# Performance work log

Hardware: AMD Instinct MI355X
Metric: run time of the kernel (lower is better)

Reference implementation:

```python
import jax, jax.numpy as jnp
import numpy as np


def setup_inputs() -> dict:
    key = jax.random.key(0)
    ks = jax.random.split(key, 5)
    B, H, W, C = 4, 64, 64, 256
    Ck = C // 8  # key/query channels = 32
    x = jax.random.normal(ks[0], (B, H, W, C), dtype=jnp.float32)
    # 1x1 conv kernels (spec_norm=False -> plain conv), Glorot-ish scaling
    Wf = jax.random.normal(ks[1], (C, Ck), dtype=jnp.float32) * (1.0 / np.sqrt(C))
    Wg = jax.random.normal(ks[2], (C, Ck), dtype=jnp.float32) * (1.0 / np.sqrt(C))
    Wh = jax.random.normal(ks[3], (C, C), dtype=jnp.float32) * (1.0 / np.sqrt(C))
    bf = jnp.zeros((Ck,), dtype=jnp.float32)
    bg = jnp.zeros((Ck,), dtype=jnp.float32)
    bh = jnp.zeros((C,), dtype=jnp.float32)
    # gamma is zero-init in the module; use a nonzero value so the attention
    # branch actually contributes to the output (as after some training).
    gamma = jnp.float32(0.5)
    return {"x": x, "Wf": Wf, "bf": bf, "Wg": Wg, "bg": bg,
            "Wh": Wh, "bh": bh, "gamma": gamma}


def reference(x, Wf, bf, Wg, bg, Wh, bh, gamma):
    B, H, W, C = x.shape
    N = H * W
    xf = x.reshape(B, N, C)  # hw_flatten of input (1x1 conv == per-pixel matmul)
    f = xf @ Wf + bf         # [B, N, Ck] keys
    g = xf @ Wg + bg         # [B, N, Ck] queries
    h = xf @ Wh + bh         # [B, N, C]  values
    s = jnp.einsum('bqk,bnk->bqn', g, f)  # [B, N, N] scores (g @ f^T)
    b = jax.nn.softmax(s, axis=-1)
    o = jnp.einsum('bqn,bnc->bqc', b, h)  # [B, N, C]
    # in-channels == nfilters, so scale(x) = x (identity)
    y = gamma * o.reshape(B, H, W, C) + x
    return y
```

## Files before the change

### kernel.cpp

```cpp
#include <hip/hip_runtime.h>
#include <stdint.h>

#define B_ 4
#define N_ 4096
#define C_ 256
#define LOG2E 1.44269504088896340736f
#define SOFT_OFF 88.0f

typedef float f32x4 __attribute__((ext_vector_type(4)));
typedef float f32x16 __attribute__((ext_vector_type(16)));
typedef short s16x8 __attribute__((ext_vector_type(8)));
typedef __bf16 bf16x8 __attribute__((ext_vector_type(8)));
typedef _Float16 f16x8 __attribute__((ext_vector_type(8)));

static __device__ __forceinline__ unsigned short f2bf(float f) {
    union { float f; uint32_t u; } v; v.f = f;
    return (unsigned short)((v.u + 0x7FFFu + ((v.u >> 16) & 1u)) >> 16);
}
static __device__ __forceinline__ unsigned short f2bf_rh(float f) {
    union { float f; uint32_t u; } v; v.f = f;
    return (unsigned short)((v.u + 0x8000u) >> 16);
}

__global__ __launch_bounds__(256) void wprep(
    const float* __restrict__ Wf, const float* __restrict__ Wg,
    const float* __restrict__ Wh, _Float16* __restrict__ WT)
{
    __shared__ float tile[64][33];
    const int t = blockIdx.x, kc = blockIdx.y, tid = threadIdx.x;
    const float* src; int stride;
    if (t == 0)      { src = Wf;                stride = 32;  }
    else if (t == 1) { src = Wg;                stride = 32;  }
    else             { src = Wh + (t - 2) * 32; stride = 256; }

    const int c = tid & 31, a = tid >> 5;
    #pragma unroll
    for (int p = 0; p < 8; p++) {
        int kk = p * 8 + a;
        tile[kk][c] = src[(size_t)(kc * 64 + kk) * stride + c];
    }
    __syncthreads();
    const int kk = tid & 63, aa = tid >> 6;
    #pragma unroll
    for (int p = 0; p < 8; p++) {
        int cc = p * 4 + aa;
        WT[(size_t)(t * 32 + cc) * 256 + kc * 64 + kk] = (_Float16)tile[kk][cc];
    }
}

__global__ __launch_bounds__(256, 2) void proj_kernel(
    const float* __restrict__ x,
    const float* __restrict__ bfp, const float* __restrict__ bgp,
    const float* __restrict__ bhp,
    const _Float16* __restrict__ WT,
    _Float16* __restrict__ qf16, _Float16* __restrict__ kf16,
    unsigned short* __restrict__ v_frag)
{
    __shared__ __align__(16) _Float16 xs[64 * 256];
    __shared__ __align__(16) unsigned short tbuf[4][32 * 40];

    const int tid  = threadIdx.x;
    const int lane = tid & 63;
    const int wave = tid >> 6;
    const int m_   = lane & 31;
    const int k8   = lane >> 5;
    const int row0 = blockIdx.x * 64;
    const int half = blockIdx.y;
    const int b    = row0 >> 12;
    const int n0   = row0 & 4095;
    const int kt   = n0 >> 6;

    #pragma unroll
    for (int i = 0; i < 8; i++) {
        int r  = 8 * i + (tid >> 5);
        int c5 = tid & 31;
        const f32x4* src = (const f32x4*)(x + (size_t)(row0 + r) * 256 + c5 * 8);
        f32x4 a = src[0], c4 = src[1];
        f16x8 h = { (_Float16)a.x, (_Float16)a.y, (_Float16)a.z, (_Float16)a.w,
                    (_Float16)c4.x, (_Float16)c4.y, (_Float16)c4.z, (_Float16)c4.w };
        int chunk = (((r >> 5) * 32 + c5)) * 32 + ((r & 31) ^ (c5 & 7));
        *(f16x8*)(xs + chunk * 8) = h;
    }
    __syncthreads();

    const int rowsub = wave & 1;
    const int tg     = wave >> 1;
    const int ntile  = (half == 0) ? 3 : 2;
    const int t_base = (half == 0) ? tg * 3 : 6 + tg * 2;
    const _Float16* wb[3];
    #pragma unroll
    for (int t = 0; t < 3; t++)
        wb[t] = WT + (size_t)((t_base + (t < ntile ? t : 0)) * 32 + m_) * 256 + k8 * 8;

    f32x16 acc[3];
    #pragma unroll
    for (int t = 0; t < 3; t++)
        #pragma unroll
        for (int i = 0; i < 16; i++) acc[t][i] = 0.f;

    f16x8 Bb[2][4][3];
    #pragma unroll
    for (int j = 0; j < 4; j++)
        #pragma unroll
        for (int t = 0; t < 3; t++) {
            if (t >= ntile) break;
            Bb[0][j][t] = *(const f16x8*)(wb[t] + j * 16);
        }
    #pragma unroll
    for (int g4 = 0; g4 < 4; g4++) {
        const int cur = g4 & 1, nxt = cur ^ 1;
        if (g4 < 3)
            #pragma unroll
            for (int j = 0; j < 4; j++)
                #pragma unroll
                for (int t = 0; t < 3; t++) {
                    if (t >= ntile) break;
                    Bb[nxt][j][t] = *(const f16x8*)(wb[t] + (g4 * 4 + 4 + j) * 16);
                }
        #pragma unroll
        for (int j = 0; j < 4; j++) {
            int ks = g4 * 4 + j;
            f16x8 A = *(const f16x8*)(xs + ((rowsub * 32 + ks * 2 + k8) * 32
                                            + (m_ ^ ((ks * 2 + k8) & 7))) * 8);
            #pragma unroll
            for (int t = 0; t < 3; t++) {
                if (t >= ntile) break;
                acc[t] = __builtin_amdgcn_mfma_f32_32x32x16_f16(A, Bb[cur][j][t],
                                                                acc[t], 0, 0, 0);
            }
        }
    }

    #pragma unroll
    for (int t = 0; t < 3; t++) {
        if (t >= ntile) break;
        const int tile = t_base + t;
        if (tile < 2) {
            float bias = (tile == 0) ? bfp[m_] : bgp[m_];
            _Float16* dst = (tile == 0) ? kf16 : qf16;
            #pragma unroll
            for (int r = 0; r < 16; r++) {
                int m = (r & 3) + 8 * (r >> 2) + 4 * k8;
                int row = row0 + rowsub * 32 + m;
                dst[(size_t)row * 32 + m_] = (_Float16)(acc[t][r] + bias);
            }
        } else {
            const int ht   = tile - 2;
            const int chgv = ht >> 2, chslv = ht & 3;
            float bias = bhp[ht * 32 + m_];
            unsigned short* buf = tbuf[wave];
            #pragma unroll
            for (int u = 0; u < 8; u++) {
                int r = 2 * u;
                int m = (r & 3) + 8 * (r >> 2) + 4 * k8;
                uint32_t v = (uint32_t)f2bf(acc[t][r] + bias)
                           | ((uint32_t)f2bf(acc[t][r + 1] + bias) << 16);
                *(uint32_t*)(buf + m_ * 40 + m) = v;
            }
            #pragma unroll
            for (int u = 0; u < 2; u++) {
                int idx2 = u * 64 + lane;
                int chr = idx2 >> 2, q8 = idx2 & 3;
                s16x8 vv = *(const s16x8*)(buf + chr * 40 + q8 * 8);
                int oct = rowsub * 4 + q8;
                size_t e = (((((size_t)(b * 2 + chgv) * 64 + kt) * 8 + oct) * 4
                              + chslv) * 32 + chr) * 8;
                *(s16x8*)(v_frag + e) = vv;
            }
        }
    }
}

__global__ __launch_bounds__(1024, 4) void attn_kernel(
    const _Float16* __restrict__ qf16, const _Float16* __restrict__ kf16,
    const unsigned short* __restrict__ v_frag,
    const float* __restrict__ x, const float* __restrict__ gamma_p,
    float* __restrict__ out)
{
    __shared__ __align__(16) unsigned short P_s[2][2][4096];
    __shared__ float l_s[2][4][32];

    const int tid  = threadIdx.x;
    const int lane = tid & 63;
    const int wave = tid >> 6;
    const int qsub = wave & 1;
    const int j    = wave >> 1;
    const int m_   = lane & 31;
    const int k8   = lane >> 5;
    const int qt   = blockIdx.x;
    const int b    = blockIdx.y;
    const size_t bn = (size_t)b * N_;
    const bool is_s = (wave < 8);
    const int ksl  = j;
    const int octw = ksl * 4 + (m_ >> 3);
    const int osw  = octw & 3;
    const int kofs = m_ & 7;

    const unsigned short* vb = v_frag + (size_t)(b * 2 + (j >> 2)) * 524288
                             + (j & 3) * 256 + m_ * 8;

    const int qrow = qt * 64 + qsub * 32 + m_;
    const f16x8 Aq0 = *(const f16x8*)(qf16 + (bn + qrow) * 32 + k8 * 8);
    const f16x8 Aq1 = *(const f16x8*)(qf16 + (bn + qrow) * 32 + 16 + k8 * 8);

    f16x8 Kc0 = {}, Kc1 = {};
    if (is_s) {
        const _Float16* kp = kf16 + (bn + ksl * 32 + m_) * 32;
        Kc0 = *(const f16x8*)(kp + k8 * 8);
        Kc1 = *(const f16x8*)(kp + 16 + k8 * 8);
    }
    bf16x8 Bv0[4], Bv1[4];
    #pragma unroll
    for (int ks = 0; ks < 4; ks++)
        Bv0[ks] = *(const bf16x8*)(vb + (ks * 2 + k8) * 1024);

    f32x16 acc;
    float l_acc[16];
    #pragma unroll
    for (int i = 0; i < 16; i++) { acc[i] = 0.f; l_acc[i] = 0.f; }

    for (int it = 0; it < 32; it++) {
        const int par = it & 1;
        const int itn = (it < 31) ? it + 1 : 31;
        f16x8 Kn0 = {}, Kn1 = {};
        if (is_s) {
            const _Float16* kp = kf16 + (bn + itn * 128 + ksl * 32 + m_) * 32;
            Kn0 = *(const f16x8*)(kp + k8 * 8);
            Kn1 = *(const f16x8*)(kp + 16 + k8 * 8);
            f32x16 s;
            #pragma unroll
            for (int i = 0; i < 16; i++) s[i] = 0.f;
            s = __builtin_amdgcn_mfma_f32_32x32x16_f16(Aq0, Kc0, s, 0, 0, 0);
            s = __builtin_amdgcn_mfma_f32_32x32x16_f16(Aq1, Kc1, s, 0, 0, 0);
            unsigned short* Pb = P_s[par][qsub];
            #pragma unroll
            for (int r = 0; r < 16; r++) {
                float p = __builtin_amdgcn_exp2f(fmaf(s[r], LOG2E, -SOFT_OFF));
                l_acc[r] += p;
                int q = (r & 3) + 8 * (r >> 2) + 4 * k8;
                Pb[(octw * 32 + (q ^ osw)) * 8 + kofs] = f2bf_rh(p);
            }
        }
        __syncthreads();

        const unsigned short* Pr = P_s[par][qsub];
        #pragma unroll
        for (int ks = 0; ks < 4; ks++)
            Bv1[ks] = *(const bf16x8*)(vb + (size_t)it * 16384 + 8192
                                       + (ks * 2 + k8) * 1024);
        #pragma unroll
        for (int ks = 0; ks < 4; ks++) {
            int oct = ks * 2 + k8;
            bf16x8 Ap = *(const bf16x8*)(Pr + (oct * 32 + (m_ ^ (oct & 3))) * 8);
            acc = __builtin_amdgcn_mfma_f32_32x32x16_bf16(Ap, Bv0[ks], acc, 0, 0, 0);
        }
        #pragma unroll
        for (int ks = 0; ks < 4; ks++) {
            int oct = 8 + ks * 2 + k8;
            bf16x8 Ap = *(const bf16x8*)(Pr + (oct * 32 + (m_ ^ (oct & 3))) * 8);
            acc = __builtin_amdgcn_mfma_f32_32x32x16_bf16(Ap, Bv1[ks], acc, 0, 0, 0);
        }
        #pragma unroll
        for (int ks = 0; ks < 4; ks++)
            Bv0[ks] = *(const bf16x8*)(vb + (size_t)itn * 16384
                                       + (ks * 2 + k8) * 1024);
        if (is_s) { Kc0 = Kn0; Kc1 = Kn1; }
    }

    if (is_s) {
        #pragma unroll
        for (int off = 1; off < 32; off <<= 1)
            #pragma unroll
            for (int r = 0; r < 16; r++)
                l_acc[r] += __shfl_xor(l_acc[r], off, 64);
        if (m_ == 0) {
            #pragma unroll
            for (int r = 0; r < 16; r++) {
                int q = (r & 3) + 8 * (r >> 2) + 4 * k8;
                l_s[qsub][ksl][q] = l_acc[r];
            }
        }
    }
    __syncthreads();

    const float gamma = *gamma_p;
    #pragma unroll
    for (int r = 0; r < 16; r++) {
        int q = (r & 3) + 8 * (r >> 2) + 4 * k8;
        float l = l_s[qsub][0][q] + l_s[qsub][1][q]
                + l_s[qsub][2][q] + l_s[qsub][3][q];
        size_t idx = (bn + qt * 64 + qsub * 32 + q) * 256 + j * 32 + m_;
        out[idx] = gamma * (acc[r] / l) + x[idx];
    }
}

extern "C" void kernel_launch(void* const* d_in, const int* in_sizes, int n_in,
                              void* d_out, int out_size, void* d_ws, size_t ws_size,
                              hipStream_t stream) {
    const float* x   = (const float*)d_in[0];
    const float* Wf  = (const float*)d_in[1];
    const float* bfp = (const float*)d_in[2];
    const float* Wg  = (const float*)d_in[3];
    const float* bgp = (const float*)d_in[4];
    const float* Wh  = (const float*)d_in[5];
    const float* bhp = (const float*)d_in[6];
    const float* gam = (const float*)d_in[7];
    float* out = (float*)d_out;

    unsigned char* ws = (unsigned char*)d_ws;
    const size_t MB = 1 << 20;
    _Float16* WT    = (_Float16*)(ws);
    _Float16* qf16  = (_Float16*)(ws + 1 * MB);
    _Float16* kf16  = (_Float16*)(ws + 2 * MB);
    unsigned short* v_frag = (unsigned short*)(ws + 3 * MB);

    wprep<<<dim3(10, 4), dim3(256), 0, stream>>>(Wf, Wg, Wh, WT);
    proj_kernel<<<dim3(256, 2), dim3(256), 0, stream>>>(
        x, bfp, bgp, bhp, WT, qf16, kf16, v_frag);
    attn_kernel<<<dim3(64, 4), dim3(1024), 0, stream>>>(
        qf16, kf16, v_frag, x, gam, out);
}
```

Baseline: 149.8 us.

## Software-pipeline score computation one tile ahead, alternating between two wave groups

Score/exp work for the next key tile now runs while the PV MFMAs for the current tile execute. It writes into the other half of the double-buffered P tile, with a prologue that precomputes tile 0. The score duty alternates between the two 8-wave groups, so all 16 waves share the exp work instead of only the first 8. The row-sum reduction is extended to all waves with a vectorized layout. The aim is to hide the score/softmax latency behind the PV matmul and balance load across waves, at the cost of more complex index logic and a K prefetch two tiles ahead.

```diff
diff --git a/kernel.cpp b/kernel.cpp
--- a/kernel.cpp
+++ b/kernel.cpp
@@ -178,20 +178,20 @@
     float* __restrict__ out)
 {
     __shared__ __align__(16) unsigned short P_s[2][2][4096];
-    __shared__ float l_s[2][4][32];
+    __shared__ __align__(16) float l_s[2][32][8];
 
     const int tid  = threadIdx.x;
     const int lane = tid & 63;
     const int wave = tid >> 6;
     const int qsub = wave & 1;
     const int j    = wave >> 1;
+    const int ksl  = j & 3;
+    const int sgrp = j >> 2;
     const int m_   = lane & 31;
     const int k8   = lane >> 5;
     const int qt   = blockIdx.x;
     const int b    = blockIdx.y;
     const size_t bn = (size_t)b * N_;
-    const bool is_s = (wave < 8);
-    const int ksl  = j;
     const int octw = ksl * 4 + (m_ >> 3);
     const int osw  = octw & 3;
     const int kofs = m_ & 7;
@@ -203,9 +203,30 @@
     const f16x8 Aq0 = *(const f16x8*)(qf16 + (bn + qrow) * 32 + k8 * 8);
     const f16x8 Aq1 = *(const f16x8*)(qf16 + (bn + qrow) * 32 + 16 + k8 * 8);
 
-    f16x8 Kc0 = {}, Kc1 = {};
-    if (is_s) {
-        const _Float16* kp = kf16 + (bn + ksl * 32 + m_) * 32;
+    const _Float16* kp0 = kf16 + (bn + sgrp * 128 + ksl * 32 + m_) * 32;
+    f16x8 Kc0 = *(const f16x8*)(kp0 + k8 * 8);
+    f16x8 Kc1 = *(const f16x8*)(kp0 + 16 + k8 * 8);
+
+    f32x16 acc;
+    float l_acc[16];
+    #pragma unroll
+    for (int i = 0; i < 16; i++) { acc[i] = 0.f; l_acc[i] = 0.f; }
+
+    if (sgrp == 0) {
+        f32x16 s;
+        #pragma unroll
+        for (int i = 0; i < 16; i++) s[i] = 0.f;
+        s = __builtin_amdgcn_mfma_f32_32x32x16_f16(Aq0, Kc0, s, 0, 0, 0);
+        s = __builtin_amdgcn_mfma_f32_32x32x16_f16(Aq1, Kc1, s, 0, 0, 0);
+        unsigned short* Pb = P_s[0][qsub];
+        #pragma unroll
+        for (int r = 0; r < 16; r++) {
+            float p = __builtin_amdgcn_exp2f(fmaf(s[r], LOG2E, -SOFT_OFF));
+            l_acc[r] += p;
+            int q = (r & 3) + 8 * (r >> 2) + 4 * k8;
+            Pb[(octw * 32 + (q ^ osw)) * 8 + kofs] = f2bf_rh(p);
+        }
+        const _Float16* kp = kf16 + (bn + 2 * 128 + ksl * 32 + m_) * 32;
         Kc0 = *(const f16x8*)(kp + k8 * 8);
         Kc1 = *(const f16x8*)(kp + 16 + k8 * 8);
     }
@@ -213,26 +234,36 @@
     #pragma unroll
     for (int ks = 0; ks < 4; ks++)
         Bv0[ks] = *(const bf16x8*)(vb + (ks * 2 + k8) * 1024);
-
-    f32x16 acc;
-    float l_acc[16];
-    #pragma unroll
-    for (int i = 0; i < 16; i++) { acc[i] = 0.f; l_acc[i] = 0.f; }
+    __syncthreads();
 
     for (int it = 0; it < 32; it++) {
         const int par = it & 1;
         const int itn = (it < 31) ? it + 1 : 31;
-        f16x8 Kn0 = {}, Kn1 = {};
-        if (is_s) {
-            const _Float16* kp = kf16 + (bn + itn * 128 + ksl * 32 + m_) * 32;
-            Kn0 = *(const f16x8*)(kp + k8 * 8);
-            Kn1 = *(const f16x8*)(kp + 16 + k8 * 8);
-            f32x16 s;
+        const bool duty = (((it + 1) & 1) == sgrp) && (it < 31);
+
+        #pragma unroll
+        for (int ks = 0; ks < 4; ks++)
+            Bv1[ks] = *(const bf16x8*)(vb + (size_t)it * 16384 + 8192
+                                       + (ks * 2 + k8) * 1024);
+
+        f32x16 s;
+        if (duty) {
             #pragma unroll
             for (int i = 0; i < 16; i++) s[i] = 0.f;
             s = __builtin_amdgcn_mfma_f32_32x32x16_f16(Aq0, Kc0, s, 0, 0, 0);
             s = __builtin_amdgcn_mfma_f32_32x32x16_f16(Aq1, Kc1, s, 0, 0, 0);
-            unsigned short* Pb = P_s[par][qsub];
+        }
+
+        const unsigned short* Pr = P_s[par][qsub];
+        #pragma unroll
+        for (int ks = 0; ks < 4; ks++) {
+            int oct = ks * 2 + k8;
+            bf16x8 Ap = *(const bf16x8*)(Pr + (oct * 32 + (m_ ^ (oct & 3))) * 8);
+            acc = __builtin_amdgcn_mfma_f32_32x32x16_bf16(Ap, Bv0[ks], acc, 0, 0, 0);
+        }
+
+        if (duty) {
+            unsigned short* Pb = P_s[par ^ 1][qsub];
             #pragma unroll
             for (int r = 0; r < 16; r++) {
                 float p = __builtin_amdgcn_exp2f(fmaf(s[r], LOG2E, -SOFT_OFF));
@@ -240,20 +271,12 @@
                 int q = (r & 3) + 8 * (r >> 2) + 4 * k8;
                 Pb[(octw * 32 + (q ^ osw)) * 8 + kofs] = f2bf_rh(p);
             }
-        }
-        __syncthreads();
-
-        const unsigned short* Pr = P_s[par][qsub];
-        #pragma unroll
-        for (int ks = 0; ks < 4; ks++)
-            Bv1[ks] = *(const bf16x8*)(vb + (size_t)it * 16384 + 8192
-                                       + (ks * 2 + k8) * 1024);
-        #pragma unroll
-        for (int ks = 0; ks < 4; ks++) {
-            int oct = ks * 2 + k8;
-            bf16x8 Ap = *(const bf16x8*)(Pr + (oct * 32 + (m_ ^ (oct & 3))) * 8);
-            acc = __builtin_amdgcn_mfma_f32_32x32x16_bf16(Ap, Bv0[ks], acc, 0, 0, 0);
-        }
+            int kt3 = (it + 3 < 32) ? (it + 3) : 31;
+            const _Float16* kp = kf16 + (bn + (size_t)kt3 * 128 + ksl * 32 + m_) * 32;
+            Kc0 = *(const f16x8*)(kp + k8 * 8);
+            Kc1 = *(const f16x8*)(kp + 16 + k8 * 8);
+        }
+
         #pragma unroll
         for (int ks = 0; ks < 4; ks++) {
             int oct = 8 + ks * 2 + k8;
@@ -264,21 +287,19 @@
         for (int ks = 0; ks < 4; ks++)
             Bv0[ks] = *(const bf16x8*)(vb + (size_t)itn * 16384
                                        + (ks * 2 + k8) * 1024);
-        if (is_s) { Kc0 = Kn0; Kc1 = Kn1; }
-    }
-
-    if (is_s) {
-        #pragma unroll
-        for (int off = 1; off < 32; off <<= 1)
-            #pragma unroll
-            for (int r = 0; r < 16; r++)
-                l_acc[r] += __shfl_xor(l_acc[r], off, 64);
-        if (m_ == 0) {
-            #pragma unroll
-            for (int r = 0; r < 16; r++) {
-                int q = (r & 3) + 8 * (r >> 2) + 4 * k8;
-                l_s[qsub][ksl][q] = l_acc[r];
-            }
+        __syncthreads();
+    }
+
+    #pragma unroll
+    for (int off = 1; off < 32; off <<= 1)
+        #pragma unroll
+        for (int r = 0; r < 16; r++)
+            l_acc[r] += __shfl_xor(l_acc[r], off, 64);
+    if (m_ == 0) {
+        #pragma unroll
+        for (int r = 0; r < 16; r++) {
+            int q = (r & 3) + 8 * (r >> 2) + 4 * k8;
+            l_s[qsub][q][j] = l_acc[r];
         }
     }
     __syncthreads();
@@ -287,8 +308,10 @@
     #pragma unroll
     for (int r = 0; r < 16; r++) {
         int q = (r & 3) + 8 * (r >> 2) + 4 * k8;
-        float l = l_s[qsub][0][q] + l_s[qsub][1][q]
-                + l_s[qsub][2][q] + l_s[qsub][3][q];
+        f32x4 la = *(const f32x4*)(&l_s[qsub][q][0]);
+        f32x4 lb = *(const f32x4*)(&l_s[qsub][q][4]);
+        float l = ((la.x + la.y) + (la.z + la.w))
+                + ((lb.x + lb.y) + (lb.z + lb.w));
         size_t idx = (bn + qt * 64 + qsub * 32 + q) * 256 + j * 32 + m_;
         out[idx] = gamma * (acc[r] / l) + x[idx];
     }
```

Measured after the change: 176.3 us. 1.18x slower.

## Keep softmax probabilities in registers via transposed score MFMA, split keys across waves

Applied to the files above, without the earlier changes.

The attention kernel now computes S^T (K as the A operand) so each lane's exponentiated scores map directly onto the A-fragment layout of the PV MFMA. This removes the LDS round trip for P and the per-iteration __syncthreads. Each wave owns a key slice and accumulates 4 channel tiles, and the partial outputs are reduced across the 4 key-slice waves through LDS at the end. Blocks shrink to 512 threads covering 32 queries, and the V fragment write layout in the projection kernel is permuted to match the new operand ordering. The costs are more accumulator registers per wave, a serialized end-of-kernel reduction with several barriers, and lower occupancy.

```diff
diff --git a/kernel.cpp b/kernel.cpp
--- a/kernel.cpp
+++ b/kernel.cpp
@@ -9,6 +9,7 @@
 
 typedef float f32x4 __attribute__((ext_vector_type(4)));
 typedef float f32x16 __attribute__((ext_vector_type(16)));
+typedef short s16x4 __attribute__((ext_vector_type(4)));
 typedef short s16x8 __attribute__((ext_vector_type(8)));
 typedef __bf16 bf16x8 __attribute__((ext_vector_type(8)));
 typedef _Float16 f16x8 __attribute__((ext_vector_type(8)));
@@ -160,9 +161,13 @@
             #pragma unroll
             for (int u = 0; u < 2; u++) {
                 int idx2 = u * 64 + lane;
-                int chr = idx2 >> 2, q8 = idx2 & 3;
-                s16x8 vv = *(const s16x8*)(buf + chr * 40 + q8 * 8);
-                int oct = rowsub * 4 + q8;
+                int chr = idx2 >> 2, sl = idx2 & 3;
+                int gg = sl >> 1, hh = sl & 1;
+                s16x4 lo = *(const s16x4*)(buf + chr * 40 + gg * 16 + hh * 4);
+                s16x4 hi = *(const s16x4*)(buf + chr * 40 + gg * 16 + hh * 4 + 8);
+                s16x8 vv = { lo[0], lo[1], lo[2], lo[3],
+                             hi[0], hi[1], hi[2], hi[3] };
+                int oct = rowsub * 4 + sl;
                 size_t e = (((((size_t)(b * 2 + chgv) * 64 + kt) * 8 + oct) * 4
                               + chslv) * 32 + chr) * 8;
                 *(s16x8*)(v_frag + e) = vv;
@@ -171,126 +176,143 @@
     }
 }
 
-__global__ __launch_bounds__(1024, 4) void attn_kernel(
+__global__ __launch_bounds__(512, 2) void attn_kernel(
     const _Float16* __restrict__ qf16, const _Float16* __restrict__ kf16,
     const unsigned short* __restrict__ v_frag,
     const float* __restrict__ x, const float* __restrict__ gamma_p,
     float* __restrict__ out)
 {
-    __shared__ __align__(16) unsigned short P_s[2][2][4096];
-    __shared__ float l_s[2][4][32];
+    __shared__ __align__(16) float acc_s[32][256];
+    __shared__ float l_sl[4][32];
 
     const int tid  = threadIdx.x;
     const int lane = tid & 63;
     const int wave = tid >> 6;
-    const int qsub = wave & 1;
-    const int j    = wave >> 1;
+    const int ks   = wave & 3;
+    const int cg   = wave >> 2;
     const int m_   = lane & 31;
     const int k8   = lane >> 5;
     const int qt   = blockIdx.x;
-    const int b    = blockIdx.y;
+    const int qsub = blockIdx.y;
+    const int b    = blockIdx.z;
     const size_t bn = (size_t)b * N_;
-    const bool is_s = (wave < 8);
-    const int ksl  = j;
-    const int octw = ksl * 4 + (m_ >> 3);
-    const int osw  = octw & 3;
-    const int kofs = m_ & 7;
-
-    const unsigned short* vb = v_frag + (size_t)(b * 2 + (j >> 2)) * 524288
-                             + (j & 3) * 256 + m_ * 8;
 
     const int qrow = qt * 64 + qsub * 32 + m_;
     const f16x8 Aq0 = *(const f16x8*)(qf16 + (bn + qrow) * 32 + k8 * 8);
     const f16x8 Aq1 = *(const f16x8*)(qf16 + (bn + qrow) * 32 + 16 + k8 * 8);
 
-    f16x8 Kc0 = {}, Kc1 = {};
-    if (is_s) {
-        const _Float16* kp = kf16 + (bn + ksl * 32 + m_) * 32;
-        Kc0 = *(const f16x8*)(kp + k8 * 8);
-        Kc1 = *(const f16x8*)(kp + 16 + k8 * 8);
-    }
-    bf16x8 Bv0[4], Bv1[4];
-    #pragma unroll
-    for (int ks = 0; ks < 4; ks++)
-        Bv0[ks] = *(const bf16x8*)(vb + (ks * 2 + k8) * 1024);
-
-    f32x16 acc;
-    float l_acc[16];
-    #pragma unroll
-    for (int i = 0; i < 16; i++) { acc[i] = 0.f; l_acc[i] = 0.f; }
+    const _Float16* kbase = kf16 + (bn + ks * 32 + m_) * 32;
+    f16x8 Kc0 = *(const f16x8*)(kbase + k8 * 8);
+    f16x8 Kc1 = *(const f16x8*)(kbase + 16 + k8 * 8);
+
+    const unsigned short* vb = v_frag + (size_t)(b * 2 + cg) * 524288 + m_ * 8;
+    const int oct0 = ks * 4 + k8, oct1 = ks * 4 + 2 + k8;
+    const int off0 = (oct0 >> 3) * 8192 + (oct0 & 7) * 1024;
+    const int off1 = (oct1 >> 3) * 8192 + (oct1 & 7) * 1024;
+
+    f32x16 acc[4];
+    #pragma unroll
+    for (int t = 0; t < 4; t++)
+        #pragma unroll
+        for (int i = 0; i < 16; i++) acc[t][i] = 0.f;
+    float l_acc = 0.f;
 
     for (int it = 0; it < 32; it++) {
-        const int par = it & 1;
-        const int itn = (it < 31) ? it + 1 : 31;
-        f16x8 Kn0 = {}, Kn1 = {};
-        if (is_s) {
-            const _Float16* kp = kf16 + (bn + itn * 128 + ksl * 32 + m_) * 32;
-            Kn0 = *(const f16x8*)(kp + k8 * 8);
-            Kn1 = *(const f16x8*)(kp + 16 + k8 * 8);
-            f32x16 s;
-            #pragma unroll
-            for (int i = 0; i < 16; i++) s[i] = 0.f;
-            s = __builtin_amdgcn_mfma_f32_32x32x16_f16(Aq0, Kc0, s, 0, 0, 0);
-            s = __builtin_amdgcn_mfma_f32_32x32x16_f16(Aq1, Kc1, s, 0, 0, 0);
-            unsigned short* Pb = P_s[par][qsub];
-            #pragma unroll
-            for (int r = 0; r < 16; r++) {
-                float p = __builtin_amdgcn_exp2f(fmaf(s[r], LOG2E, -SOFT_OFF));
-                l_acc[r] += p;
-                int q = (r & 3) + 8 * (r >> 2) + 4 * k8;
-                Pb[(octw * 32 + (q ^ osw)) * 8 + kofs] = f2bf_rh(p);
-            }
+        const unsigned short* vit = vb + (size_t)it * 16384;
+        bf16x8 Bv0[4];
+        #pragma unroll
+        for (int t = 0; t < 4; t++)
+            Bv0[t] = *(const bf16x8*)(vit + t * 256 + off0);
+
+        f32x16 s2;
+        #pragma unroll
+        for (int i = 0; i < 16; i++) s2[i] = 0.f;
+        s2 = __builtin_amdgcn_mfma_f32_32x32x16_f16(Kc0, Aq0, s2, 0, 0, 0);
+        s2 = __builtin_amdgcn_mfma_f32_32x32x16_f16(Kc1, Aq1, s2, 0, 0, 0);
+
+        bf16x8 Bv1[4];
+        #pragma unroll
+        for (int t = 0; t < 4; t++)
+            Bv1[t] = *(const bf16x8*)(vit + t * 256 + off1);
+
+        {
+            int itn = (it < 31) ? it + 1 : 31;
+            Kc0 = *(const f16x8*)(kbase + itn * 4096 + k8 * 8);
+            Kc1 = *(const f16x8*)(kbase + itn * 4096 + 16 + k8 * 8);
+        }
+
+        float p0 = __builtin_amdgcn_exp2f(fmaf(s2[0], LOG2E, -SOFT_OFF));
+        float p1 = __builtin_amdgcn_exp2f(fmaf(s2[1], LOG2E, -SOFT_OFF));
+        float p2 = __builtin_amdgcn_exp2f(fmaf(s2[2], LOG2E, -SOFT_OFF));
+        float p3 = __builtin_amdgcn_exp2f(fmaf(s2[3], LOG2E, -SOFT_OFF));
+        float p4 = __builtin_amdgcn_exp2f(fmaf(s2[4], LOG2E, -SOFT_OFF));
+        float p5 = __builtin_amdgcn_exp2f(fmaf(s2[5], LOG2E, -SOFT_OFF));
+        float p6 = __builtin_amdgcn_exp2f(fmaf(s2[6], LOG2E, -SOFT_OFF));
+        float p7 = __builtin_amdgcn_exp2f(fmaf(s2[7], LOG2E, -SOFT_OFF));
+        l_acc += ((p0 + p1) + (p2 + p3)) + ((p4 + p5) + (p6 + p7));
+        union { uint32_t u[4]; bf16x8 v; } f0;
+        f0.u[0] = (uint32_t)f2bf_rh(p0) | ((uint32_t)f2bf_rh(p1) << 16);
+        f0.u[1] = (uint32_t)f2bf_rh(p2) | ((uint32_t)f2bf_rh(p3) << 16);
+        f0.u[2] = (uint32_t)f2bf_rh(p4) | ((uint32_t)f2bf_rh(p5) << 16);
+        f0.u[3] = (uint32_t)f2bf_rh(p6) | ((uint32_t)f2bf_rh(p7) << 16);
+        #pragma unroll
+        for (int t = 0; t < 4; t++)
+            acc[t] = __builtin_amdgcn_mfma_f32_32x32x16_bf16(f0.v, Bv0[t],
+                                                             acc[t], 0, 0, 0);
+
+        float q0 = __builtin_amdgcn_exp2f(fmaf(s2[8],  LOG2E, -SOFT_OFF));
+        float q1 = __builtin_amdgcn_exp2f(fmaf(s2[9],  LOG2E, -SOFT_OFF));
+        float q2 = __builtin_amdgcn_exp2f(fmaf(s2[10], LOG2E, -SOFT_OFF));
+        float q3 = __builtin_amdgcn_exp2f(fmaf(s2[11], LOG2E, -SOFT_OFF));
+        float q4 = __builtin_amdgcn_exp2f(fmaf(s2[12], LOG2E, -SOFT_OFF));
+        float q5 = __builtin_amdgcn_exp2f(fmaf(s2[13], LOG2E, -SOFT_OFF));
+        float q6 = __builtin_amdgcn_exp2f(fmaf(s2[14], LOG2E, -SOFT_OFF));
+        float q7 = __builtin_amdgcn_exp2f(fmaf(s2[15], LOG2E, -SOFT_OFF));
+        l_acc += ((q0 + q1) + (q2 + q3)) + ((q4 + q5) + (q6 + q7));
+        union { uint32_t u[4]; bf16x8 v; } f1;
+        f1.u[0] = (uint32_t)f2bf_rh(q0) | ((uint32_t)f2bf_rh(q1) << 16);
+        f1.u[1] = (uint32_t)f2bf_rh(q2) | ((uint32_t)f2bf_rh(q3) << 16);
+        f1.u[2] = (uint32_t)f2bf_rh(q4) | ((uint32_t)f2bf_rh(q5) << 16);
+        f1.u[3] = (uint32_t)f2bf_rh(q6) | ((uint32_t)f2bf_rh(q7) << 16);
+        #pragma unroll
+        for (int t = 0; t < 4; t++)
+            acc[t] = __builtin_amdgcn_mfma_f32_32x32x16_bf16(f1.v, Bv1[t],
+                                                             acc[t], 0, 0, 0);
+    }
+
+    float l_full = l_acc + __shfl_xor(l_acc, 32);
+    if (cg == 0 && lane < 32) l_sl[ks][m_] = l_full;
+
+    #pragma unroll
+    for (int rd = 0; rd < 4; rd++) {
+        if (ks == rd) {
+            #pragma unroll
+            for (int t = 0; t < 4; t++)
+                #pragma unroll
+                for (int r = 0; r < 16; r++) {
+                    int q = (r & 3) + 8 * (r >> 2) + 4 * k8;
+                    float* pp = &acc_s[q][cg * 128 + t * 32 + m_];
+                    if (rd == 0) *pp = acc[t][r];
+                    else         *pp += acc[t][r];
+                }
         }
         __syncthreads();
-
-        const unsigned short* Pr = P_s[par][qsub];
-        #pragma unroll
-        for (int ks = 0; ks < 4; ks++)
-            Bv1[ks] = *(const bf16x8*)(vb + (size_t)it * 16384 + 8192
-                                       + (ks * 2 + k8) * 1024);
-        #pragma unroll
-        for (int ks = 0; ks < 4; ks++) {
-            int oct = ks * 2 + k8;
-            bf16x8 Ap = *(const bf16x8*)(Pr + (oct * 32 + (m_ ^ (oct & 3))) * 8);
-            acc = __builtin_amdgcn_mfma_f32_32x32x16_bf16(Ap, Bv0[ks], acc, 0, 0, 0);
-        }
-        #pragma unroll
-        for (int ks = 0; ks < 4; ks++) {
-            int oct = 8 + ks * 2 + k8;
-            bf16x8 Ap = *(const bf16x8*)(Pr + (oct * 32 + (m_ ^ (oct & 3))) * 8);
-            acc = __builtin_amdgcn_mfma_f32_32x32x16_bf16(Ap, Bv1[ks], acc, 0, 0, 0);
-        }
-        #pragma unroll
-        for (int ks = 0; ks < 4; ks++)
-            Bv0[ks] = *(const bf16x8*)(vb + (size_t)itn * 16384
-                                       + (ks * 2 + k8) * 1024);
-        if (is_s) { Kc0 = Kn0; Kc1 = Kn1; }
-    }
-
-    if (is_s) {
-        #pragma unroll
-        for (int off = 1; off < 32; off <<= 1)
-            #pragma unroll
-            for (int r = 0; r < 16; r++)
-                l_acc[r] += __shfl_xor(l_acc[r], off, 64);
-        if (m_ == 0) {
-            #pragma unroll
-            for (int r = 0; r < 16; r++) {
-                int q = (r & 3) + 8 * (r >> 2) + 4 * k8;
-                l_s[qsub][ksl][q] = l_acc[r];
-            }
-        }
-    }
-    __syncthreads();
+    }
 
     const float gamma = *gamma_p;
     #pragma unroll
-    for (int r = 0; r < 16; r++) {
-        int q = (r & 3) + 8 * (r >> 2) + 4 * k8;
-        float l = l_s[qsub][0][q] + l_s[qsub][1][q]
-                + l_s[qsub][2][q] + l_s[qsub][3][q];
-        size_t idx = (bn + qt * 64 + qsub * 32 + q) * 256 + j * 32 + m_;
-        out[idx] = gamma * (acc[r] / l) + x[idx];
+    for (int i = 0; i < 4; i++) {
+        int q = wave * 4 + i;
+        float l = (l_sl[0][q] + l_sl[1][q]) + (l_sl[2][q] + l_sl[3][q]);
+        f32x4 a4 = *(const f32x4*)&acc_s[q][lane * 4];
+        size_t idx = (bn + qt * 64 + qsub * 32 + q) * 256 + lane * 4;
+        f32x4 xv = *(const f32x4*)(x + idx);
+        f32x4 o;
+        o.x = gamma * (a4.x / l) + xv.x;
+        o.y = gamma * (a4.y / l) + xv.y;
+        o.z = gamma * (a4.z / l) + xv.z;
+        o.w = gamma * (a4.w / l) + xv.w;
+        *(f32x4*)(out + idx) = o;
     }
 }
 
@@ -317,6 +339,6 @@
     wprep<<<dim3(10, 4), dim3(256), 0, stream>>>(Wf, Wg, Wh, WT);
     proj_kernel<<<dim3(256, 2), dim3(256), 0, stream>>>(
         x, bfp, bgp, bhp, WT, qf16, kf16, v_frag);
-    attn_kernel<<<dim3(64, 4), dim3(1024), 0, stream>>>(
+    attn_kernel<<<dim3(64, 2, 4), dim3(512), 0, stream>>>(
         qf16, kf16, v_frag, x, gam, out);
 }
```

Result: slower. 160.3 us (+7.0%).
